# Kernel tuning notes

Hardware: AMD Instinct MI355X
Metric: run time of the kernel (lower is better)

## Reference

```python
import jax, jax.numpy as jnp
import numpy as np

NS, NV = 32, 8                      # scalar / vector multiplicities
N_NODES, N_EDGES, N_EF = 10000, 100000, 64
W1, W2, W3, W4 = NS*NS, NV*NV, NS*NV, NV*NS   # path weight sizes
WNUM = W1 + W2 + W3 + W4            # 1600
D_NODE = NS + 3*NV                  # 56

def mish(x):
    return x * jnp.tanh(jax.nn.softplus(x))

def setup_inputs() -> dict:
    key = jax.random.key(0)
    ks = jax.random.split(key, 8)
    return dict(
        node_attr=jax.random.normal(ks[0], (N_NODES, D_NODE), jnp.float32),
        edge_index=jax.random.randint(ks[1], (2, N_EDGES), 0, N_NODES),
        edge_attr=jax.random.normal(ks[2], (N_EDGES, N_EF), jnp.float32),
        edge_sh=jax.random.normal(ks[3], (N_EDGES, 4), jnp.float32),
        fc1_w=jax.random.normal(ks[4], (N_EF, N_EF), jnp.float32) / np.sqrt(N_EF),
        fc1_b=jnp.zeros((N_EF,), jnp.float32),
        fc2_w=jax.random.normal(ks[5], (N_EF, WNUM), jnp.float32) / np.sqrt(N_EF),
        fc2_b=jnp.zeros((WNUM,), jnp.float32),
        bn_gamma_s=jnp.ones((NS,), jnp.float32),
        bn_beta_s=jnp.zeros((NS,), jnp.float32),
        bn_gamma_v=jnp.ones((NV,), jnp.float32),
    )

def reference(node_attr, edge_index, edge_attr, edge_sh,
              fc1_w, fc1_b, fc2_w, fc2_b,
              bn_gamma_s, bn_beta_s, bn_gamma_v):
    edge_src, edge_dst = edge_index[0], edge_index[1]
    # edge-conditioned TP weights: Linear -> Mish -> Linear
    w = mish(edge_attr @ fc1_w + fc1_b) @ fc2_w + fc2_b            # [E, WNUM]
    w1 = w[:, :W1].reshape(-1, NS, NS)           # 0e x 0e -> 0e
    w2 = w[:, W1:W1+W2].reshape(-1, NV, NV)      # 1o x 0e -> 1o
    w3 = w[:, W1+W2:W1+W2+W3].reshape(-1, NS, NV)  # 0e x 1o -> 1o
    w4 = w[:, W1+W2+W3:].reshape(-1, NV, NS)     # 1o x 1o -> 0e
    # gather destination node features
    x = node_attr[edge_dst]
    s = x[:, :NS]                                # [E,NS]
    v = x[:, NS:].reshape(-1, NV, 3)             # [E,NV,3]
    sh0 = edge_sh[:, 0]                          # [E]
    sh1 = edge_sh[:, 1:4]                        # [E,3]
    # path normalization: 1/sqrt(total fan-in per output irrep) = 1/sqrt(NS+NV)
    a = 1.0 / np.sqrt(float(NS + NV))
    dot = jnp.einsum('euc,ec->eu', v, sh1) / np.sqrt(3.0)  # CG(1,1,0)
    out_s = a * (jnp.einsum('eu,euw->ew', s * sh0[:, None], w1)
               + jnp.einsum('eu,euw->ew', dot, w4))          # [E,NS]
    out_v = a * (jnp.einsum('euc,euw->ewc', v * sh0[:, None, None], w2)
               + jnp.einsum('eu,ec,euw->ewc', s, sh1, w3))   # [E,NV,3]
    tp = jnp.concatenate([out_s, out_v.reshape(-1, 3*NV)], axis=-1)  # [E,D_NODE]
    # scatter-mean over edge_src
    summ = jax.ops.segment_sum(tp, edge_src, num_segments=N_NODES)
    cnt = jax.ops.segment_sum(jnp.ones((N_EDGES,), tp.dtype), edge_src, num_segments=N_NODES)
    out = summ / jnp.maximum(cnt, 1.0)[:, None]
    # residual (in/out irreps equal -> pad is a no-op)
    out = out + node_attr
    # e3nn-style BatchNorm (training batch stats), eps=1e-4, component norm
    eps = 1e-4
    os = out[:, :NS]
    ov = out[:, NS:].reshape(-1, NV, 3)
    mu = os.mean(axis=0)
    osc = os - mu
    var = (osc * osc).mean(axis=0)
    os_n = osc * jax.lax.rsqrt(var + eps) * bn_gamma_s + bn_beta_s
    vn = (ov * ov).mean(axis=-1).mean(axis=0)                 # [NV]
    ov_n = ov * (jax.lax.rsqrt(vn + eps) * bn_gamma_v)[None, :, None]
    return jnp.concatenate([os_n, ov_n.reshape(-1, 3*NV)], axis=-1)
```

## Files before the change

kernel.cpp:

```cpp
#include <hip/hip_runtime.h>
#include <stdint.h>

#define NNODES 10000
#define NEDGES 100000
#define DNODE 56
#define JTOT 1600
#define HBLK 391
#define TBLK 400

typedef __attribute__((ext_vector_type(8))) short short8;
typedef __attribute__((ext_vector_type(4))) float floatx4;

__device__ __forceinline__ unsigned short f2bf(float f) {
  unsigned u = __float_as_uint(f);
  u = u + 0x7fffu + ((u >> 16) & 1u);
  return (unsigned short)(u >> 16);
}

__device__ __forceinline__ float mishf(float x) {
  float e = __expf(x);
  float z = 1.f + e; z = z * z;
  float t = (z - 1.f) / (z + 1.f);
  t = (x > 40.f) ? 1.f : t;
  return x * t;
}

__global__ __launch_bounds__(256) void k_hidtr(const float* __restrict__ ea,
                                               const float* __restrict__ fc1w,
                                               const float* __restrict__ fc1b,
                                               const float* __restrict__ fc2w,
                                               const int* __restrict__ eidx,
                                               int* __restrict__ cntn,
                                               unsigned short* __restrict__ hb,
                                               unsigned short* __restrict__ G) {
  int bid = blockIdx.x;
  if (bid >= HBLK) {
    int idx = (bid - HBLK) * 256 + threadIdx.x;
    if (idx < 64 * JTOT) {
      int j = idx >> 6, k = idx & 63;
      G[idx] = f2bf(fc2w[k * JTOT + j]);
    }
    return;
  }
  int e = bid * 256 + threadIdx.x;
  if (e >= NEDGES) return;
  atomicAdd(&cntn[eidx[e]], 1);
  float a[64];
  const float4* row = (const float4*)(ea + (size_t)e * 64);
  #pragma unroll
  for (int i = 0; i < 16; i++) {
    float4 t = row[i];
    a[4*i] = t.x; a[4*i+1] = t.y; a[4*i+2] = t.z; a[4*i+3] = t.w;
  }
  for (int jb = 0; jb < 64; jb += 8) {
    float acc[8];
    #pragma unroll
    for (int i = 0; i < 8; i++) acc[i] = fc1b[jb + i];
    #pragma unroll
    for (int k = 0; k < 64; k++) {
      #pragma unroll
      for (int i = 0; i < 8; i++) acc[i] = fmaf(a[k], fc1w[k*64 + jb + i], acc[i]);
    }
    unsigned pk[4];
    #pragma unroll
    for (int i = 0; i < 4; i++) {
      unsigned lo = f2bf(mishf(acc[2*i]));
      unsigned hi = f2bf(mishf(acc[2*i+1]));
      pk[i] = lo | (hi << 16);
    }
    *(uint4*)(hb + (size_t)e*64 + jb) = make_uint4(pk[0], pk[1], pk[2], pk[3]);
  }
}

__global__ __launch_bounds__(1024) void k_scan(const int* __restrict__ cntn,
                                               int* __restrict__ offs,
                                               int* __restrict__ cursor) {
  __shared__ int ts[1024];
  int t = threadIdx.x;
  int base = t * 10;
  int loc[10]; int s = 0;
  #pragma unroll
  for (int i = 0; i < 10; i++) {
    int idx = base + i;
    int v = (idx < NNODES) ? cntn[idx] : 0;
    loc[i] = s; s += v;
  }
  ts[t] = s;
  __syncthreads();
  for (int off = 1; off < 1024; off <<= 1) {
    int v = (t >= off) ? ts[t - off] : 0;
    __syncthreads();
    ts[t] += v;
    __syncthreads();
  }
  int excl = (t == 0) ? 0 : ts[t - 1];
  #pragma unroll
  for (int i = 0; i < 10; i++) {
    int idx = base + i;
    if (idx < NNODES) { int o = excl + loc[i]; offs[idx] = o; cursor[idx] = o; }
  }
  if (t == 1023) offs[NNODES] = ts[1023];
}

__global__ __launch_bounds__(256, 3) void k_tp(
    const unsigned short* __restrict__ hb,
    const unsigned short* __restrict__ G,
    const float* __restrict__ fc2b,
    const int* __restrict__ eidx,
    const float* __restrict__ node_attr,
    const float* __restrict__ edge_sh,
    int* __restrict__ cursor,
    float* __restrict__ tp) {
  __shared__ short Gs[2][2][1024];
  __shared__ float b2s[JTOT];
  __shared__ float Wt4[4][64 * 32];
  __shared__ int pos_s[4][32];
  const int tid = threadIdx.x;
  const int wave = tid >> 6, lane = tid & 63;
  for (int i = tid; i < JTOT; i += 256) b2s[i] = fc2b[i];

  const int e0w = blockIdx.x * 128 + wave * 32;
  float* Wt = &Wt4[wave][0];
  {
    int el = lane & 31, hh = lane >> 5;
    int e = e0w + el;
    bool valid = e < NEDGES;
    int dst = valid ? eidx[NEDGES + e] : 0;
    const float* na = node_attr + (size_t)dst * DNODE;
    if (hh == 0) {
      pos_s[wave][el] = valid ? atomicAdd(&cursor[eidx[e]], 1) : 0;
      #pragma unroll
      for (int u = 0; u < 32; u += 4) {
        float4 t = valid ? *(const float4*)(na + u) : make_float4(0.f,0.f,0.f,0.f);
        Wt[(u+0)*32 + el] = t.x;
        Wt[(u+1)*32 + el] = t.y;
        Wt[(u+2)*32 + el] = t.z;
        Wt[(u+3)*32 + el] = t.w;
      }
    } else {
      float4 sh = valid ? *(const float4*)(edge_sh + 4*(size_t)e) : make_float4(0.f,0.f,0.f,0.f);
      const float rs3 = 0.57735026918962576f;
      #pragma unroll
      for (int u = 0; u < 8; u++) {
        float v0 = valid ? na[32 + u*3 + 0] : 0.f;
        float v1 = valid ? na[32 + u*3 + 1] : 0.f;
        float v2 = valid ? na[32 + u*3 + 2] : 0.f;
        Wt[(32 + u*3 + 0)*32 + el] = v0;
        Wt[(32 + u*3 + 1)*32 + el] = v1;
        Wt[(32 + u*3 + 2)*32 + el] = v2;
        Wt[(56 + u)*32 + el] = (v0*sh.y + v1*sh.z + v2*sh.w) * rs3;
      }
    }
  }

  const int col = lane & 15, rg = lane >> 4, rgh = rg >> 1;
  float sh0c[2], sh1c[2][3];
  bool vld[2];
  short8 bfrag[2][2];
  const short8 zfrag = {0,0,0,0,0,0,0,0};
  #pragma unroll
  for (int nt = 0; nt < 2; nt++) {
    int e = e0w + nt*16 + col;
    bool v = e < NEDGES; vld[nt] = v;
    if (v) {
      float4 sh = *(const float4*)(edge_sh + 4*(size_t)e);
      sh0c[nt] = sh.x; sh1c[nt][0] = sh.y; sh1c[nt][1] = sh.z; sh1c[nt][2] = sh.w;
      const unsigned short* hp = hb + (size_t)e * 64;
      bfrag[nt][0] = *(const short8*)(hp + rg*8);
      bfrag[nt][1] = *(const short8*)(hp + 32 + rg*8);
    } else {
      sh0c[nt] = 0.f; sh1c[nt][0] = sh1c[nt][1] = sh1c[nt][2] = 0.f;
      bfrag[nt][0] = zfrag; bfrag[nt][1] = zfrag;
    }
  }

  float sacc[2][8], vacc[2][12];
  #pragma unroll
  for (int nt = 0; nt < 2; nt++) {
    #pragma unroll
    for (int i = 0; i < 8; i++) sacc[nt][i] = 0.f;
    #pragma unroll
    for (int i = 0; i < 12; i++) vacc[nt][i] = 0.f;
  }

  auto stage = [&](int c) {
    int t = tid >> 7, gt = tid & 127;
    int jp = gt >> 3, g = gt & 7;
    int gsw = (gt & ~7) | (g ^ (jp & 7));
    short8 v = *(const short8*)(G + (size_t)c*2048 + tid*8);
    *(short8*)(&Gs[c&1][t][gsw*8]) = v;
  };

  const int g0 = (rg ^ (col & 7)) * 8;
  const int g1 = ((rg + 4) ^ (col & 7)) * 8;

  stage(0);
  __syncthreads();

  #pragma unroll 1
  for (int c = 0; c < 50; c++) {
    if (c < 49) stage(c + 1);
    #pragma unroll
    for (int t = 0; t < 2; t++) {
      const int jt = c*2 + t;
      const short* gb = &Gs[c&1][t][0];
      short8 x0 = *(const short8*)(gb + col*64 + g0);
      short8 x1 = *(const short8*)(gb + col*64 + g1);
      float4 bb = *(const float4*)&b2s[jt*16 + rg*4];
      floatx4 acc[2];
      #pragma unroll
      for (int nt = 0; nt < 2; nt++) {
        floatx4 cc = {bb.x, bb.y, bb.z, bb.w};
        cc = __builtin_amdgcn_mfma_f32_16x16x32_bf16(x0, bfrag[nt][0], cc, 0, 0, 0);
        cc = __builtin_amdgcn_mfma_f32_16x16x32_bf16(x1, bfrag[nt][1], cc, 0, 0, 0);
        acc[nt] = cc;
      }
      if (jt < 64) {
        const int u = jt >> 1, p = jt & 1;
        #pragma unroll
        for (int nt = 0; nt < 2; nt++) {
          float cf = Wt[u*32 + nt*16 + col] * sh0c[nt];
          #pragma unroll
          for (int r = 0; r < 4; r++)
            sacc[nt][p*4+r] = fmaf(cf, acc[nt][r], sacc[nt][p*4+r]);
        }
      } else if (jt < 68) {
        const int u = (jt - 64)*2 + rgh;
        #pragma unroll
        for (int nt = 0; nt < 2; nt++) {
          #pragma unroll
          for (int c3 = 0; c3 < 3; c3++) {
            float cf = Wt[(32 + u*3 + c3)*32 + nt*16 + col] * sh0c[nt];
            #pragma unroll
            for (int r = 0; r < 4; r++)
              vacc[nt][c3*4+r] = fmaf(cf, acc[nt][r], vacc[nt][c3*4+r]);
          }
        }
      } else if (jt < 84) {
        const int u = (jt - 68)*2 + rgh;
        #pragma unroll
        for (int nt = 0; nt < 2; nt++) {
          float sv = Wt[u*32 + nt*16 + col];
          #pragma unroll
          for (int c3 = 0; c3 < 3; c3++) {
            float cf = sv * sh1c[nt][c3];
            #pragma unroll
            for (int r = 0; r < 4; r++)
              vacc[nt][c3*4+r] = fmaf(cf, acc[nt][r], vacc[nt][c3*4+r]);
          }
        }
      } else {
        const int u = (jt - 84) >> 1, p = jt & 1;
        #pragma unroll
        for (int nt = 0; nt < 2; nt++) {
          float cf = Wt[(56 + u)*32 + nt*16 + col];
          #pragma unroll
          for (int r = 0; r < 4; r++)
            sacc[nt][p*4+r] = fmaf(cf, acc[nt][r], sacc[nt][p*4+r]);
        }
      }
    }
    __syncthreads();
  }

  const float ascale = 0.15811388300841897f;
  #pragma unroll
  for (int nt = 0; nt < 2; nt++) {
    int el = nt*16 + col;
    float* rowp = tp + (size_t)pos_s[wave][el] * DNODE;
    if (vld[nt]) {
      #pragma unroll
      for (int p = 0; p < 2; p++) {
        float4 v = make_float4(ascale*sacc[nt][p*4+0], ascale*sacc[nt][p*4+1],
                               ascale*sacc[nt][p*4+2], ascale*sacc[nt][p*4+3]);
        *(float4*)(rowp + p*16 + rg*4) = v;
      }
    }
    float vtot[12];
    #pragma unroll
    for (int k = 0; k < 12; k++)
      vtot[k] = (vacc[nt][k] + __shfl_xor(vacc[nt][k], 32)) * ascale;
    if (rg < 2 && vld[nt]) {
      float tmp[12];
      #pragma unroll
      for (int c3 = 0; c3 < 3; c3++)
        #pragma unroll
        for (int r = 0; r < 4; r++) tmp[r*3 + c3] = vtot[c3*4 + r];
      #pragma unroll
      for (int j = 0; j < 3; j++)
        *(float4*)(rowp + 32 + (rg & 1)*12 + j*4) = *(float4*)&tmp[j*4];
    }
  }
}

__global__ __launch_bounds__(256) void k_gather(const float* __restrict__ tp,
                                                const int* __restrict__ offs,
                                                const float* __restrict__ node_attr,
                                                float* __restrict__ pre,
                                                float* __restrict__ pstat) {
  __shared__ float redS[4*64], redQ[4*64];
  int t = threadIdx.x, wave = t >> 6, lane = t & 63;
  int gw = blockIdx.x * 4 + wave;
  const int W = 640 * 4;
  int off = (lane < DNODE) ? lane : 0;
  float ssum = 0.f, ssq = 0.f;
  for (int n = gw; n < NNODES; n += W) {
    int beg = offs[n], end = offs[n+1];
    float acc = 0.f;
    int i = beg;
    for (; i + 4 <= end; i += 4) {
      float v0 = tp[(size_t)(i+0)*DNODE + off];
      float v1 = tp[(size_t)(i+1)*DNODE + off];
      float v2 = tp[(size_t)(i+2)*DNODE + off];
      float v3 = tp[(size_t)(i+3)*DNODE + off];
      acc += (v0 + v1) + (v2 + v3);
    }
    for (; i < end; i++) acc += tp[(size_t)i*DNODE + off];
    int c = end - beg; if (c < 1) c = 1;
    float m = acc / (float)c + node_attr[(size_t)n*DNODE + off];
    if (lane < DNODE) { pre[(size_t)n*DNODE + lane] = m; ssum += m; ssq += m*m; }
  }
  redS[wave*64 + lane] = ssum;
  redQ[wave*64 + lane] = ssq;
  __syncthreads();
  if (wave == 0 && lane < DNODE) {
    float a = redS[lane] + redS[64+lane] + redS[128+lane] + redS[192+lane];
    float b = redQ[lane] + redQ[64+lane] + redQ[128+lane] + redQ[192+lane];
    pstat[(size_t)blockIdx.x*112 + lane] = a;
    pstat[(size_t)blockIdx.x*112 + 56 + lane] = b;
  }
}

__global__ __launch_bounds__(256) void k_stats(const float* __restrict__ pstat,
                                               float* __restrict__ stats) {
  int f = blockIdx.x * 4 + (threadIdx.x >> 6);
  int lane = threadIdx.x & 63;
  float v = 0.f;
  for (int b = lane; b < 640; b += 64) v += pstat[(size_t)b*112 + f];
  #pragma unroll
  for (int o = 32; o; o >>= 1) v += __shfl_xor(v, o);
  if (lane == 0) stats[f] = v;
}

__global__ __launch_bounds__(256) void k_norm(const float* __restrict__ pre,
                                              const float* __restrict__ stats,
                                              const float* __restrict__ gs,
                                              const float* __restrict__ bs,
                                              const float* __restrict__ gv,
                                              float* __restrict__ out) {
  int idx = blockIdx.x * 256 + threadIdx.x;
  if (idx >= NNODES * DNODE) return;
  int n = idx / DNODE;
  int d = idx - n * DNODE;
  float val = pre[idx];
  const float invN = 1.f / (float)NNODES;
  float res;
  if (d < 32) {
    float mu = stats[d] * invN;
    float var = stats[56 + d] * invN - mu * mu;
    res = (val - mu) * rsqrtf(var + 1e-4f) * gs[d] + bs[d];
  } else {
    int wi = (d - 32) / 3;
    float vn = (stats[56 + 32 + wi*3] + stats[56 + 32 + wi*3 + 1] +
                stats[56 + 32 + wi*3 + 2]) * (invN / 3.f);
    res = val * rsqrtf(vn + 1e-4f) * gv[wi];
  }
  out[idx] = res;
}

extern "C" void kernel_launch(void* const* d_in, const int* in_sizes, int n_in,
                              void* d_out, int out_size, void* d_ws, size_t ws_size,
                              hipStream_t stream) {
  const float* node_attr = (const float*)d_in[0];
  const int*   eidx      = (const int*)d_in[1];
  const float* edge_attr = (const float*)d_in[2];
  const float* edge_sh   = (const float*)d_in[3];
  const float* fc1w      = (const float*)d_in[4];
  const float* fc1b      = (const float*)d_in[5];
  const float* fc2w      = (const float*)d_in[6];
  const float* fc2b      = (const float*)d_in[7];
  const float* gs        = (const float*)d_in[8];
  const float* bs        = (const float*)d_in[9];
  const float* gv        = (const float*)d_in[10];

  float* ws = (float*)d_ws;
  float* tp    = ws;
  float* pre   = ws + 5600000;
  float* stats = ws + 6160000;
  float* pstat = ws + 6160128;
  int*   cntn  = (int*)(ws + 6231808);
  int*   offs  = (int*)(ws + 6241808);
  int*   cursor= (int*)(ws + 6251816);
  unsigned short* G  = (unsigned short*)(ws + 6261816);
  unsigned short* hb = (unsigned short*)(ws + 6313016);

  hipMemsetAsync(cntn, 0, (size_t)10000 * 4, stream);
  k_hidtr<<<HBLK + TBLK, 256, 0, stream>>>(edge_attr, fc1w, fc1b, fc2w, eidx, cntn, hb, G);
  k_scan<<<1, 1024, 0, stream>>>(cntn, offs, cursor);
  k_tp<<<782, 256, 0, stream>>>(hb, G, fc2b, eidx, node_attr, edge_sh, cursor, tp);
  k_gather<<<640, 256, 0, stream>>>(tp, offs, node_attr, pre, pstat);
  k_stats<<<28, 256, 0, stream>>>(pstat, stats);
  k_norm<<<(NNODES * DNODE + 255) / 256, 256, 0, stream>>>(pre, stats, gs, bs, gv, (float*)d_out);
}
```

Baseline: 241.3 us.

## Move fc1 to bf16 MFMA and stream pre-swizzled fc2 weights via async LDS loads

The first linear layer now runs as a per-block bf16 MFMA over 128 edges with LDS-staged transposed weights, replacing the per-thread scalar FMA loop. The fc2 weight tensor is pre-swizzled at conversion time so the TP kernel can fetch 4-tile chunks with global_load_lds directly into LDS. Each block starts at a different chunk to spread L2 traffic. The per-edge node features are stored as bf16 in LDS to cut LDS use and allow occupancy 4, at some loss of precision in the coefficients.

```diff
diff --git a/kernel.cpp b/kernel.cpp
--- a/kernel.cpp
+++ b/kernel.cpp
@@ -5,7 +5,7 @@
 #define NEDGES 100000
 #define DNODE 56
 #define JTOT 1600
-#define HBLK 391
+#define EBLK 782
 #define TBLK 400
 
 typedef __attribute__((ext_vector_type(8))) short short8;
@@ -15,6 +15,9 @@
   unsigned u = __float_as_uint(f);
   u = u + 0x7fffu + ((u >> 16) & 1u);
   return (unsigned short)(u >> 16);
+}
+__device__ __forceinline__ float bf2f(unsigned short u) {
+  return __uint_as_float(((unsigned)u) << 16);
 }
 
 __device__ __forceinline__ float mishf(float x) {
@@ -25,50 +28,109 @@
   return x * t;
 }
 
-__global__ __launch_bounds__(256) void k_hidtr(const float* __restrict__ ea,
-                                               const float* __restrict__ fc1w,
-                                               const float* __restrict__ fc1b,
-                                               const float* __restrict__ fc2w,
-                                               const int* __restrict__ eidx,
-                                               int* __restrict__ cntn,
-                                               unsigned short* __restrict__ hb,
-                                               unsigned short* __restrict__ G) {
-  int bid = blockIdx.x;
-  if (bid >= HBLK) {
-    int idx = (bid - HBLK) * 256 + threadIdx.x;
+__device__ __forceinline__ void async_ld16(void* lds, const void* gp) {
+  __builtin_amdgcn_global_load_lds(
+      (const __attribute__((address_space(1))) unsigned int*)gp,
+      (__attribute__((address_space(3))) unsigned int*)lds, 16, 0, 0);
+}
+
+__global__ __launch_bounds__(256, 4) void k_hidtr(const float* __restrict__ ea,
+                                                  const float* __restrict__ fc1w,
+                                                  const float* __restrict__ fc1b,
+                                                  const float* __restrict__ fc2w,
+                                                  const int* __restrict__ eidx,
+                                                  int* __restrict__ cntn,
+                                                  unsigned short* __restrict__ hb,
+                                                  unsigned short* __restrict__ G) {
+  const int bid = blockIdx.x, tid = threadIdx.x;
+  if (bid >= EBLK) {
+    int idx = (bid - EBLK) * 256 + tid;
     if (idx < 64 * JTOT) {
-      int j = idx >> 6, k = idx & 63;
+      int jt = idx >> 10, r = idx & 1023;
+      int c = r >> 6, w = r & 63;
+      int slot = w >> 3, s = w & 7;
+      int g = slot ^ (c & 7);
+      int k = g * 8 + s;
+      int j = jt * 16 + c;
       G[idx] = f2bf(fc2w[k * JTOT + j]);
     }
     return;
   }
-  int e = bid * 256 + threadIdx.x;
-  if (e >= NEDGES) return;
-  atomicAdd(&cntn[eidx[e]], 1);
-  float a[64];
-  const float4* row = (const float4*)(ea + (size_t)e * 64);
-  #pragma unroll
-  for (int i = 0; i < 16; i++) {
-    float4 t = row[i];
-    a[4*i] = t.x; a[4*i+1] = t.y; a[4*i+2] = t.z; a[4*i+3] = t.w;
-  }
-  for (int jb = 0; jb < 64; jb += 8) {
-    float acc[8];
-    #pragma unroll
-    for (int i = 0; i < 8; i++) acc[i] = fc1b[jb + i];
-    #pragma unroll
-    for (int k = 0; k < 64; k++) {
-      #pragma unroll
-      for (int i = 0; i < 8; i++) acc[i] = fmaf(a[k], fc1w[k*64 + jb + i], acc[i]);
-    }
-    unsigned pk[4];
-    #pragma unroll
-    for (int i = 0; i < 4; i++) {
-      unsigned lo = f2bf(mishf(acc[2*i]));
-      unsigned hi = f2bf(mishf(acc[2*i+1]));
-      pk[i] = lo | (hi << 16);
-    }
-    *(uint4*)(hb + (size_t)e*64 + jb) = make_uint4(pk[0], pk[1], pk[2], pk[3]);
+  __shared__ unsigned short T[64 * 72];
+  __shared__ unsigned short E[128 * 72];
+  __shared__ float b1s[64];
+  const int e0 = bid * 128;
+  if (tid < 128) {
+    int e = e0 + tid;
+    if (e < NEDGES) atomicAdd(&cntn[eidx[e]], 1);
+  }
+  if (tid < 64) b1s[tid] = fc1b[tid];
+  #pragma unroll
+  for (int it = 0; it < 4; it++) {
+    int q = tid + 256 * it;
+    int k = q >> 4, j4 = (q & 15) * 4;
+    float4 v = *(const float4*)(fc1w + (size_t)q * 4);
+    T[(j4+0)*72 + k] = f2bf(v.x);
+    T[(j4+1)*72 + k] = f2bf(v.y);
+    T[(j4+2)*72 + k] = f2bf(v.z);
+    T[(j4+3)*72 + k] = f2bf(v.w);
+  }
+  #pragma unroll
+  for (int it = 0; it < 8; it++) {
+    int q = tid + 256 * it;
+    int e = q >> 4, k4 = (q & 15) * 4;
+    int ge = e0 + e;
+    float4 v = (ge < NEDGES) ? *(const float4*)(ea + (size_t)ge * 64 + k4)
+                             : make_float4(0.f, 0.f, 0.f, 0.f);
+    ushort4 p;
+    p.x = f2bf(v.x); p.y = f2bf(v.y); p.z = f2bf(v.z); p.w = f2bf(v.w);
+    *(ushort4*)(&E[e*72 + k4]) = p;
+  }
+  __syncthreads();
+
+  const int wave = tid >> 6, lane = tid & 63, col = lane & 15, rg = lane >> 4;
+  short8 bf[2][2];
+  #pragma unroll
+  for (int nt = 0; nt < 2; nt++) {
+    int er = wave*32 + nt*16 + col;
+    bf[nt][0] = *(const short8*)(&E[er*72 + rg*8]);
+    bf[nt][1] = *(const short8*)(&E[er*72 + 32 + rg*8]);
+  }
+  floatx4 acc[4][2];
+  #pragma unroll
+  for (int jt = 0; jt < 4; jt++) {
+    int j = jt*16 + col;
+    short8 a0 = *(const short8*)(&T[j*72 + rg*8]);
+    short8 a1 = *(const short8*)(&T[j*72 + 32 + rg*8]);
+    float4 bb = *(const float4*)(&b1s[jt*16 + rg*4]);
+    #pragma unroll
+    for (int nt = 0; nt < 2; nt++) {
+      floatx4 c = {bb.x, bb.y, bb.z, bb.w};
+      c = __builtin_amdgcn_mfma_f32_16x16x32_bf16(a0, bf[nt][0], c, 0, 0, 0);
+      c = __builtin_amdgcn_mfma_f32_16x16x32_bf16(a1, bf[nt][1], c, 0, 0, 0);
+      acc[jt][nt] = c;
+    }
+  }
+  #pragma unroll
+  for (int jt = 0; jt < 4; jt++)
+    #pragma unroll
+    for (int nt = 0; nt < 2; nt++) {
+      ushort4 p;
+      p.x = f2bf(mishf(acc[jt][nt][0]));
+      p.y = f2bf(mishf(acc[jt][nt][1]));
+      p.z = f2bf(mishf(acc[jt][nt][2]));
+      p.w = f2bf(mishf(acc[jt][nt][3]));
+      *(ushort4*)(&E[(wave*32 + nt*16 + col)*72 + jt*16 + rg*4]) = p;
+    }
+  #pragma unroll
+  for (int it = 0; it < 4; it++) {
+    int g = it*64 + lane;
+    int r = g >> 3, c = g & 7;
+    int ge = e0 + wave*32 + r;
+    if (ge < NEDGES) {
+      short8 v = *(const short8*)(&E[(wave*32 + r)*72 + c*8]);
+      *(short8*)(hb + (size_t)ge*64 + c*8) = v;
+    }
   }
 }
 
@@ -102,7 +164,7 @@
   if (t == 1023) offs[NNODES] = ts[1023];
 }
 
-__global__ __launch_bounds__(256, 3) void k_tp(
+__global__ __launch_bounds__(256, 4) void k_tp(
     const unsigned short* __restrict__ hb,
     const unsigned short* __restrict__ G,
     const float* __restrict__ fc2b,
@@ -111,16 +173,16 @@
     const float* __restrict__ edge_sh,
     int* __restrict__ cursor,
     float* __restrict__ tp) {
-  __shared__ short Gs[2][2][1024];
+  __shared__ short Gs[2][4 * 1024];
+  __shared__ unsigned short wls[4][64 * 32];
   __shared__ float b2s[JTOT];
-  __shared__ float Wt4[4][64 * 32];
   __shared__ int pos_s[4][32];
   const int tid = threadIdx.x;
   const int wave = tid >> 6, lane = tid & 63;
   for (int i = tid; i < JTOT; i += 256) b2s[i] = fc2b[i];
 
   const int e0w = blockIdx.x * 128 + wave * 32;
-  float* Wt = &Wt4[wave][0];
+  unsigned short* Wt = &wls[wave][0];
   {
     int el = lane & 31, hh = lane >> 5;
     int e = e0w + el;
@@ -131,11 +193,11 @@
       pos_s[wave][el] = valid ? atomicAdd(&cursor[eidx[e]], 1) : 0;
       #pragma unroll
       for (int u = 0; u < 32; u += 4) {
-        float4 t = valid ? *(const float4*)(na + u) : make_float4(0.f,0.f,0.f,0.f);
-        Wt[(u+0)*32 + el] = t.x;
-        Wt[(u+1)*32 + el] = t.y;
-        Wt[(u+2)*32 + el] = t.z;
-        Wt[(u+3)*32 + el] = t.w;
+        float4 v = valid ? *(const float4*)(na + u) : make_float4(0.f,0.f,0.f,0.f);
+        Wt[(u+0)*32 + el] = f2bf(v.x);
+        Wt[(u+1)*32 + el] = f2bf(v.y);
+        Wt[(u+2)*32 + el] = f2bf(v.z);
+        Wt[(u+3)*32 + el] = f2bf(v.w);
       }
     } else {
       float4 sh = valid ? *(const float4*)(edge_sh + 4*(size_t)e) : make_float4(0.f,0.f,0.f,0.f);
@@ -145,15 +207,17 @@
         float v0 = valid ? na[32 + u*3 + 0] : 0.f;
         float v1 = valid ? na[32 + u*3 + 1] : 0.f;
         float v2 = valid ? na[32 + u*3 + 2] : 0.f;
-        Wt[(32 + u*3 + 0)*32 + el] = v0;
-        Wt[(32 + u*3 + 1)*32 + el] = v1;
-        Wt[(32 + u*3 + 2)*32 + el] = v2;
-        Wt[(56 + u)*32 + el] = (v0*sh.y + v1*sh.z + v2*sh.w) * rs3;
+        Wt[(32 + u*3 + 0)*32 + el] = f2bf(v0);
+        Wt[(32 + u*3 + 1)*32 + el] = f2bf(v1);
+        Wt[(32 + u*3 + 2)*32 + el] = f2bf(v2);
+        Wt[(56 + u)*32 + el] = f2bf((v0*sh.y + v1*sh.z + v2*sh.w) * rs3);
       }
     }
   }
 
   const int col = lane & 15, rg = lane >> 4, rgh = rg >> 1;
+  const int g0 = (rg ^ (col & 7)) * 8;
+  const int g1 = ((rg + 4) ^ (col & 7)) * 8;
   float sh0c[2], sh1c[2][3];
   bool vld[2];
   short8 bfrag[2][2];
@@ -183,43 +247,42 @@
     for (int i = 0; i < 12; i++) vacc[nt][i] = 0.f;
   }
 
-  auto stage = [&](int c) {
-    int t = tid >> 7, gt = tid & 127;
-    int jp = gt >> 3, g = gt & 7;
-    int gsw = (gt & ~7) | (g ^ (jp & 7));
-    short8 v = *(const short8*)(G + (size_t)c*2048 + tid*8);
-    *(short8*)(&Gs[c&1][t][gsw*8]) = v;
+  auto stage = [&](int ch, int b) {
+    const unsigned short* gsrc = G + (size_t)ch * 4096 + tid * 8;
+    #pragma unroll
+    for (int i = 0; i < 2; i++)
+      async_ld16(&Gs[b][(i*256 + wave*64) * 8], gsrc + i*256*8);
   };
 
-  const int g0 = (rg ^ (col & 7)) * 8;
-  const int g1 = ((rg + 4) ^ (col & 7)) * 8;
-
-  stage(0);
+  const int cc0 = blockIdx.x % 25;
+  stage(cc0, 0);
   __syncthreads();
 
+  int buf = 0;
   #pragma unroll 1
-  for (int c = 0; c < 50; c++) {
-    if (c < 49) stage(c + 1);
-    #pragma unroll
-    for (int t = 0; t < 2; t++) {
-      const int jt = c*2 + t;
-      const short* gb = &Gs[c&1][t][0];
+  for (int cc = 0; cc < 25; cc++) {
+    int c = cc0 + cc; if (c >= 25) c -= 25;
+    if (cc < 24) { int cn = c + 1; if (cn >= 25) cn = 0; stage(cn, buf ^ 1); }
+    #pragma unroll
+    for (int t = 0; t < 4; t++) {
+      const int jt = c * 4 + t;
+      const short* gb = &Gs[buf][t * 1024];
       short8 x0 = *(const short8*)(gb + col*64 + g0);
       short8 x1 = *(const short8*)(gb + col*64 + g1);
       float4 bb = *(const float4*)&b2s[jt*16 + rg*4];
       floatx4 acc[2];
       #pragma unroll
       for (int nt = 0; nt < 2; nt++) {
-        floatx4 cc = {bb.x, bb.y, bb.z, bb.w};
-        cc = __builtin_amdgcn_mfma_f32_16x16x32_bf16(x0, bfrag[nt][0], cc, 0, 0, 0);
-        cc = __builtin_amdgcn_mfma_f32_16x16x32_bf16(x1, bfrag[nt][1], cc, 0, 0, 0);
-        acc[nt] = cc;
+        floatx4 a = {bb.x, bb.y, bb.z, bb.w};
+        a = __builtin_amdgcn_mfma_f32_16x16x32_bf16(x0, bfrag[nt][0], a, 0, 0, 0);
+        a = __builtin_amdgcn_mfma_f32_16x16x32_bf16(x1, bfrag[nt][1], a, 0, 0, 0);
+        acc[nt] = a;
       }
       if (jt < 64) {
         const int u = jt >> 1, p = jt & 1;
         #pragma unroll
         for (int nt = 0; nt < 2; nt++) {
-          float cf = Wt[u*32 + nt*16 + col] * sh0c[nt];
+          float cf = bf2f(Wt[u*32 + nt*16 + col]) * sh0c[nt];
           #pragma unroll
           for (int r = 0; r < 4; r++)
             sacc[nt][p*4+r] = fmaf(cf, acc[nt][r], sacc[nt][p*4+r]);
@@ -229,37 +292,38 @@
         #pragma unroll
         for (int nt = 0; nt < 2; nt++) {
           #pragma unroll
-          for (int c3 = 0; c3 < 3; c3++) {
-            float cf = Wt[(32 + u*3 + c3)*32 + nt*16 + col] * sh0c[nt];
+          for (int q = 0; q < 3; q++) {
+            float cf = bf2f(Wt[(32 + u*3 + q)*32 + nt*16 + col]) * sh0c[nt];
             #pragma unroll
             for (int r = 0; r < 4; r++)
-              vacc[nt][c3*4+r] = fmaf(cf, acc[nt][r], vacc[nt][c3*4+r]);
+              vacc[nt][q*4+r] = fmaf(cf, acc[nt][r], vacc[nt][q*4+r]);
           }
         }
       } else if (jt < 84) {
         const int u = (jt - 68)*2 + rgh;
         #pragma unroll
         for (int nt = 0; nt < 2; nt++) {
-          float sv = Wt[u*32 + nt*16 + col];
+          float sv = bf2f(Wt[u*32 + nt*16 + col]);
           #pragma unroll
-          for (int c3 = 0; c3 < 3; c3++) {
-            float cf = sv * sh1c[nt][c3];
+          for (int q = 0; q < 3; q++) {
+            float cf = sv * sh1c[nt][q];
             #pragma unroll
             for (int r = 0; r < 4; r++)
-              vacc[nt][c3*4+r] = fmaf(cf, acc[nt][r], vacc[nt][c3*4+r]);
+              vacc[nt][q*4+r] = fmaf(cf, acc[nt][r], vacc[nt][q*4+r]);
           }
         }
       } else {
         const int u = (jt - 84) >> 1, p = jt & 1;
         #pragma unroll
         for (int nt = 0; nt < 2; nt++) {
-          float cf = Wt[(56 + u)*32 + nt*16 + col];
+          float cf = bf2f(Wt[(56 + u)*32 + nt*16 + col]);
           #pragma unroll
           for (int r = 0; r < 4; r++)
             sacc[nt][p*4+r] = fmaf(cf, acc[nt][r], sacc[nt][p*4+r]);
         }
       }
     }
+    buf ^= 1;
     __syncthreads();
   }
 
@@ -283,9 +347,9 @@
     if (rg < 2 && vld[nt]) {
       float tmp[12];
       #pragma unroll
-      for (int c3 = 0; c3 < 3; c3++)
+      for (int q = 0; q < 3; q++)
         #pragma unroll
-        for (int r = 0; r < 4; r++) tmp[r*3 + c3] = vtot[c3*4 + r];
+        for (int r = 0; r < 4; r++) tmp[r*3 + q] = vtot[q*4 + r];
       #pragma unroll
       for (int j = 0; j < 3; j++)
         *(float4*)(rowp + 32 + (rg & 1)*12 + j*4) = *(float4*)&tmp[j*4];
@@ -395,7 +459,7 @@
   unsigned short* hb = (unsigned short*)(ws + 6313016);
 
   hipMemsetAsync(cntn, 0, (size_t)10000 * 4, stream);
-  k_hidtr<<<HBLK + TBLK, 256, 0, stream>>>(edge_attr, fc1w, fc1b, fc2w, eidx, cntn, hb, G);
+  k_hidtr<<<EBLK + TBLK, 256, 0, stream>>>(edge_attr, fc1w, fc1b, fc2w, eidx, cntn, hb, G);
   k_scan<<<1, 1024, 0, stream>>>(cntn, offs, cursor);
   k_tp<<<782, 256, 0, stream>>>(hb, G, fc2b, eidx, node_attr, edge_sh, cursor, tp);
   k_gather<<<640, 256, 0, stream>>>(tp, offs, node_attr, pre, pstat);
```

After: 195.9 us. -18.8%, faster.
